# Kernel optimization log

Hardware: AMD Instinct MI355X
Metric: run time of the kernel (lower is better)

The kernel has to match this reference:

```python
import jax, jax.numpy as jnp
import numpy as np

E = 1024   # embed_dim
H = 16     # num_heads
NQ = 8     # ffn_dim == n_qubits
B, S = 2, 2048


def setup_inputs() -> dict:
    key = jax.random.key(0)
    ks = jax.random.split(key, 8)
    g = lambda k, sh, sc=1.0: jax.random.normal(k, sh, jnp.float32) * sc
    return {
        "x": g(ks[0], (B, S, E)),
        "w_qkv": g(ks[1], (3 * E, E), 0.02),      # nn.Linear(E, 3E, bias=False).weight
        "w_comb": g(ks[2], (E, E), 0.02),          # combine Linear weight
        "b_comb": jnp.zeros((E,), jnp.float32),
        "gamma1": jnp.ones((E,), jnp.float32),     # norm1
        "beta1": jnp.zeros((E,), jnp.float32),
        "gamma2": jnp.ones((E,), jnp.float32),     # norm2
        "beta2": jnp.zeros((E,), jnp.float32),
        "theta": g(ks[3], (NQ,)),                  # trainable RY angles
        "w1": g(ks[4], (1, NQ), 0.3),              # linear1 weight [1, n_qubits]
        "b1": jnp.zeros((1,), jnp.float32),
    }


def _layernorm(x, g, b, eps=1e-5):
    m = jnp.mean(x, axis=-1, keepdims=True)
    v = jnp.var(x, axis=-1, keepdims=True)
    return (x - m) * jax.lax.rsqrt(v + eps) * g + b


def reference(x, w_qkv, w_comb, b_comb, gamma1, beta1, gamma2, beta2, theta, w1, b1):
    Bx, Sx, Em = x.shape
    dk = Em // H
    # ---- attention ----
    qkv = (x @ w_qkv.T).reshape(Bx, Sx, 3, H, dk)
    q = jnp.transpose(qkv[:, :, 0], (0, 2, 1, 3))  # [B,H,S,dk]
    k = jnp.transpose(qkv[:, :, 1], (0, 2, 1, 3))
    v = jnp.transpose(qkv[:, :, 2], (0, 2, 1, 3))
    scores = jnp.einsum('bhqd,bhkd->bhqk', q, k) / jnp.sqrt(jnp.float32(dk))
    probs = jax.nn.softmax(scores, axis=-1)        # dropout = identity (eval)
    out = jnp.einsum('bhqk,bhkd->bhqd', probs, v)
    out = jnp.transpose(out, (0, 2, 1, 3)).reshape(Bx, Sx, Em)
    attn = out @ w_comb.T + b_comb
    x1 = _layernorm(x + attn, gamma1, beta1)
    # ---- quantum FFN: RX(x_i) encode, RY(theta_i), <Z_i> = cos(theta_i)*cos(x_i) ----
    z = jnp.cos(x1[..., :theta.shape[0]]) * jnp.cos(theta)  # [B,S,NQ]
    ffn = z @ w1.T + b1                                      # [B,S,1], broadcasts
    return _layernorm(x1 + ffn, gamma2, beta2)
```

## Files before the change

kernel.cpp:

```cpp
#include <hip/hip_runtime.h>
#include <hip/hip_bf16.h>
#include <math.h>

typedef __bf16 bf16;
typedef bf16 bf16x8 __attribute__((ext_vector_type(8)));
typedef float f32x4 __attribute__((ext_vector_type(4)));
typedef unsigned int u32;

#define EMB 1024
#define NH 16
#define DK 64
#define SEQ 2048
#define NB 2
#define NTOK (NB*SEQ)

#define QSCALE 0.18033688011112043f

#if defined(__has_builtin)
#if __has_builtin(__builtin_amdgcn_exp2f)
#define EXP2(x) __builtin_amdgcn_exp2f(x)
#else
#define EXP2(x) exp2f(x)
#endif
#else
#define EXP2(x) exp2f(x)
#endif

__device__ __forceinline__ void gl_lds16(const void* g, void* l) {
    __builtin_amdgcn_global_load_lds(
        (const __attribute__((address_space(1))) u32*)g,
        (__attribute__((address_space(3))) u32*)l, 16, 0, 0);
}

#define SWZ(row, colblk) (((row)*64) + ((((colblk) ^ ((row)&7)))*8))

#define PSTR 72

__global__ __launch_bounds__(256) void convert3(
    const float* __restrict__ s0, const float* __restrict__ s1,
    const float* __restrict__ s2,
    bf16* __restrict__ d0, bf16* __restrict__ d1, bf16* __restrict__ d2)
{
    const float* src; bf16* dst; int n;
    switch (blockIdx.y) {
        case 0:  src = s0; dst = d0; n = NTOK*EMB;  break;
        case 1:  src = s1; dst = d1; n = 3*EMB*EMB; break;
        default: src = s2; dst = d2; n = EMB*EMB;   break;
    }
    int i = (blockIdx.x * 256 + threadIdx.x) * 4;
    if (i + 3 < n) {
        float4 v = *(const float4*)(src + i);
        dst[i+0] = (bf16)v.x; dst[i+1] = (bf16)v.y;
        dst[i+2] = (bf16)v.z; dst[i+3] = (bf16)v.w;
    }
}

template<int MODE, int BM>
__global__ __launch_bounds__(256) void gemm_bt(
    const bf16* __restrict__ Aa, const bf16* __restrict__ Bb,
    bf16* __restrict__ qb, bf16* __restrict__ kb, bf16* __restrict__ vtb,
    float* __restrict__ outc, int Kdim)
{
    constexpr int MI = BM / 32;
    __shared__ __align__(16) bf16 At[BM*64];
    __shared__ __align__(16) bf16 Bt[128*64];
    const int tid  = threadIdx.x;
    const int w    = tid >> 6, lane = tid & 63;
    const int quad = lane >> 4, l15 = lane & 15;
    const int wr   = w >> 1,   wc  = w & 1;
    const int m0 = blockIdx.y * BM, n0 = blockIdx.x * 128;
    const int lrow = lane >> 3;
    const int lswz = ((lane & 7) ^ lrow) * 8;

    f32x4 acc[MI][4] = {};

    for (int k0 = 0; k0 < Kdim; k0 += 64) {
        __syncthreads();
        for (int i = 0; i < MI; ++i) {
            int r = w*(BM/4) + i*8 + lrow;
            gl_lds16(Aa + (size_t)(m0 + r)*Kdim + k0 + lswz, At + (w*(BM/4) + i*8)*64);
        }
        for (int i = 0; i < 4; ++i) {
            int r = w*32 + i*8 + lrow;
            gl_lds16(Bb + (size_t)(n0 + r)*Kdim + k0 + lswz, Bt + (w*32 + i*8)*64);
        }
        __syncthreads();
        for (int kk = 0; kk < 2; ++kk) {
            bf16x8 a[MI], b[4];
            for (int i = 0; i < MI; ++i) {
                int row = wr*(BM/2) + i*16 + l15;
                a[i] = *(const bf16x8*)(At + SWZ(row, 4*kk + quad));
            }
            for (int j = 0; j < 4; ++j) {
                int row = wc*64 + j*16 + l15;
                b[j] = *(const bf16x8*)(Bt + SWZ(row, 4*kk + quad));
            }
            for (int i = 0; i < MI; ++i)
                for (int j = 0; j < 4; ++j)
                    acc[i][j] = __builtin_amdgcn_mfma_f32_16x16x32_bf16(a[i], b[j], acc[i][j], 0, 0, 0);
        }
    }

    for (int i = 0; i < MI; ++i) for (int j = 0; j < 4; ++j) {
        int rb  = m0 + wr*(BM/2) + i*16 + quad*4;
        int col = n0 + wc*64 + j*16 + l15;
        if (MODE == 0) {
            int c = col >> 10, h = (col >> 6) & 15, d = col & 63;
            int b_ = rb >> 11, s = rb & 2047;
            int bh = b_*NH + h;
            if (c == 2) {
                bf16 tmp[4] __attribute__((aligned(8)));
                for (int r = 0; r < 4; ++r) tmp[r] = (bf16)acc[i][j][r];
                *(ushort4*)(vtb + ((size_t)bh*DK + d)*SEQ + s) = *(ushort4*)tmp;
            } else if (c == 0) {
                for (int r = 0; r < 4; ++r)
                    qb[((size_t)bh*SEQ + s + r)*DK + d] = (bf16)(acc[i][j][r] * QSCALE);
            } else {
                for (int r = 0; r < 4; ++r)
                    kb[((size_t)bh*SEQ + s + r)*DK + d] = (bf16)acc[i][j][r];
            }
        } else {
            for (int r = 0; r < 4; ++r)
                outc[(size_t)(rb + r)*EMB + col] = acc[i][j][r];
        }
    }
}

__global__ __launch_bounds__(256) void attn_kernel(
    const bf16* __restrict__ q, const bf16* __restrict__ k,
    const bf16* __restrict__ vt, bf16* __restrict__ out)
{
    __shared__ __align__(16) bf16 QP[4*32*PSTR];
    __shared__ __align__(16) bf16 Kt0[64*64];
    __shared__ __align__(16) bf16 Kt1[64*64];
    __shared__ __align__(16) bf16 Vt0[64*64];
    __shared__ __align__(16) bf16 Vt1[64*64];

    const int tid  = threadIdx.x;
    const int w    = tid >> 6, lane = tid & 63;
    const int quad = lane >> 4, l15 = lane & 15;
    const int bh = blockIdx.y, qt = blockIdx.x;
    const int lrow = lane >> 3;
    const int lswz = ((lane & 7) ^ lrow) * 8;

    for (int i = 0; i < 4; ++i) {
        int r = w*32 + i*8 + lrow;
        gl_lds16(q + ((size_t)bh*SEQ + qt*128 + r)*DK + lswz, QP + (w*32 + i*8)*64);
    }
    asm volatile("s_waitcnt vmcnt(0)" ::: "memory");

    bf16x8 qf[2][2];
    for (int rt = 0; rt < 2; ++rt)
        for (int kk = 0; kk < 2; ++kk)
            qf[rt][kk] = *(const bf16x8*)(QP + SWZ(w*32 + rt*16 + l15, 4*kk + quad));

    bf16* Pw = QP + w * 32 * PSTR;

    f32x4 O[2][4] = {};
    float psum[2][4] = {};

    auto stage_kv = [&](int kt, bf16* Kb, bf16* Vb) {
        for (int i = 0; i < 2; ++i) {
            int r = w*16 + i*8 + lrow;
            gl_lds16(k  + ((size_t)bh*SEQ + kt*64 + r)*DK + lswz, Kb + (w*16 + i*8)*64);
            gl_lds16(vt + ((size_t)bh*DK + r)*SEQ + kt*64 + lswz, Vb + (w*16 + i*8)*64);
        }
    };

    auto compute = [&](const bf16* Kb, const bf16* Vb) {
        f32x4 sc[2][4] = {};
        for (int kk = 0; kk < 2; ++kk)
            for (int j = 0; j < 4; ++j) {
                bf16x8 b = *(const bf16x8*)(Kb + SWZ(j*16 + l15, 4*kk + quad));
                for (int rt = 0; rt < 2; ++rt)
                    sc[rt][j] = __builtin_amdgcn_mfma_f32_16x16x32_bf16(qf[rt][kk], b, sc[rt][j], 0, 0, 0);
            }
        for (int rt = 0; rt < 2; ++rt)
            for (int j = 0; j < 4; ++j)
                for (int r = 0; r < 4; ++r) {
                    float p = EXP2(sc[rt][j][r]);
                    psum[rt][r] += p;
                    Pw[(rt*16 + quad*4 + r)*PSTR + j*16 + l15] = (bf16)p;
                }
        asm volatile("s_waitcnt lgkmcnt(0)" ::: "memory");
        for (int kk = 0; kk < 2; ++kk) {
            bf16x8 vb[4];
            for (int j = 0; j < 4; ++j)
                vb[j] = *(const bf16x8*)(Vb + SWZ(j*16 + l15, 4*kk + quad));
            for (int rt = 0; rt < 2; ++rt) {
                bf16x8 a = *(const bf16x8*)(Pw + (rt*16 + l15)*PSTR + kk*32 + quad*8);
                for (int j = 0; j < 4; ++j)
                    O[rt][j] = __builtin_amdgcn_mfma_f32_16x16x32_bf16(a, vb[j], O[rt][j], 0, 0, 0);
            }
        }
    };

    stage_kv(0, Kt0, Vt0);
    for (int kt2 = 0; kt2 < SEQ/128; ++kt2) {
        __syncthreads();
        stage_kv(2*kt2 + 1, Kt1, Vt1);
        compute(Kt0, Vt0);
        __syncthreads();
        if (kt2 + 1 < SEQ/128)
            stage_kv(2*kt2 + 2, Kt0, Vt0);
        compute(Kt1, Vt1);
    }

    for (int rt = 0; rt < 2; ++rt)
        for (int r = 0; r < 4; ++r) {
            float s = psum[rt][r];
            for (int m = 1; m < 16; m <<= 1) s += __shfl_xor(s, m, 64);
            psum[rt][r] = 1.f / s;
        }

    const int b_ = bh >> 4, h = bh & 15;
    for (int rt = 0; rt < 2; ++rt)
        for (int j = 0; j < 4; ++j)
            for (int r = 0; r < 4; ++r) {
                int t   = b_*SEQ + qt*128 + w*32 + rt*16 + quad*4 + r;
                int col = h*DK + j*16 + l15;
                out[(size_t)t*EMB + col] = (bf16)(O[rt][j][r] * psum[rt][r]);
            }
}

__global__ __launch_bounds__(256) void ln_kernel(
    const float* __restrict__ x, const float* __restrict__ comb,
    const float* __restrict__ bcomb,
    const float* __restrict__ g1, const float* __restrict__ be1,
    const float* __restrict__ g2, const float* __restrict__ be2,
    const float* __restrict__ theta, const float* __restrict__ w1v,
    const float* __restrict__ b1v, float* __restrict__ out)
{
    const int t = blockIdx.x, tid = threadIdx.x;
    __shared__ float red[8];
    __shared__ float fp2[2];
    const int e0 = tid*4;

    float4 xv = *(const float4*)(x    + (size_t)t*EMB + e0);
    float4 cv = *(const float4*)(comb + (size_t)t*EMB + e0);
    float4 bv = *(const float4*)(bcomb + e0);
    float r[4] = { xv.x + cv.x + bv.x, xv.y + cv.y + bv.y,
                   xv.z + cv.z + bv.z, xv.w + cv.w + bv.w };

    float s = 0.f, ss = 0.f;
    for (int i = 0; i < 4; ++i) { s += r[i]; ss += r[i]*r[i]; }
    for (int m = 1; m < 64; m <<= 1) { s += __shfl_xor(s, m, 64); ss += __shfl_xor(ss, m, 64); }
    if ((tid & 63) == 0) { red[(tid>>6)*2] = s; red[(tid>>6)*2+1] = ss; }
    __syncthreads();
    s  = red[0] + red[2] + red[4] + red[6];
    ss = red[1] + red[3] + red[5] + red[7];
    float mean = s * (1.f/1024.f);
    float var  = ss * (1.f/1024.f) - mean*mean;
    float inv  = rsqrtf(var + 1e-5f);
    float x1[4];
    for (int i = 0; i < 4; ++i) {
        int e = e0 + i;
        x1[i] = (r[i] - mean)*inv*g1[e] + be1[e];
    }
    __syncthreads();
    if (e0 < 8) {
        float pf = 0.f;
        for (int i = 0; i < 4; ++i) {
            int e = e0 + i;
            pf += cosf(x1[i]) * cosf(theta[e]) * w1v[e];
        }
        fp2[tid] = pf;
    }
    __syncthreads();
    float f = fp2[0] + fp2[1] + b1v[0];

    float s2 = 0.f, ss2 = 0.f;
    for (int i = 0; i < 4; ++i) { float v2 = x1[i] + f; s2 += v2; ss2 += v2*v2; }
    for (int m = 1; m < 64; m <<= 1) { s2 += __shfl_xor(s2, m, 64); ss2 += __shfl_xor(ss2, m, 64); }
    if ((tid & 63) == 0) { red[(tid>>6)*2] = s2; red[(tid>>6)*2+1] = ss2; }
    __syncthreads();
    s2  = red[0] + red[2] + red[4] + red[6];
    ss2 = red[1] + red[3] + red[5] + red[7];
    float mean2 = s2 * (1.f/1024.f);
    float var2  = ss2 * (1.f/1024.f) - mean2*mean2;
    float inv2  = rsqrtf(var2 + 1e-5f);
    float4 ov;
    ov.x = ((x1[0] + f) - mean2)*inv2*g2[e0+0] + be2[e0+0];
    ov.y = ((x1[1] + f) - mean2)*inv2*g2[e0+1] + be2[e0+1];
    ov.z = ((x1[2] + f) - mean2)*inv2*g2[e0+2] + be2[e0+2];
    ov.w = ((x1[3] + f) - mean2)*inv2*g2[e0+3] + be2[e0+3];
    *(float4*)(out + (size_t)t*EMB + e0) = ov;
}

extern "C" void kernel_launch(void* const* d_in, const int* in_sizes, int n_in,
                              void* d_out, int out_size, void* d_ws, size_t ws_size,
                              hipStream_t stream)
{
    const float* x      = (const float*)d_in[0];
    const float* w_qkv  = (const float*)d_in[1];
    const float* w_comb = (const float*)d_in[2];
    const float* b_comb = (const float*)d_in[3];
    const float* g1     = (const float*)d_in[4];
    const float* be1    = (const float*)d_in[5];
    const float* g2     = (const float*)d_in[6];
    const float* be2    = (const float*)d_in[7];
    const float* theta  = (const float*)d_in[8];
    const float* w1v    = (const float*)d_in[9];
    const float* b1v    = (const float*)d_in[10];
    float* out = (float*)d_out;

    char* ws = (char*)d_ws;
    bf16*  xb     = (bf16*)(ws);
    bf16*  wqkvb  = (bf16*)(ws + ( 8u<<20));
    bf16*  wcombb = (bf16*)(ws + (14u<<20));
    bf16*  qb     = (bf16*)(ws + (16u<<20));
    bf16*  kb     = (bf16*)(ws + (24u<<20));
    bf16*  vtb    = (bf16*)(ws + (32u<<20));
    bf16*  attn   = (bf16*)(ws + (40u<<20));
    float* comb   = (float*)(ws + (16u<<20));

    convert3<<<dim3(4096, 3), 256, 0, stream>>>(x, w_qkv, w_comb, xb, wqkvb, wcombb);

    gemm_bt<0,128><<<dim3(3*EMB/128, NTOK/128), 256, 0, stream>>>(
        xb, wqkvb, qb, kb, vtb, nullptr, EMB);
    attn_kernel<<<dim3(SEQ/128, NB*NH), 256, 0, stream>>>(qb, kb, vtb, attn);
    gemm_bt<1,64><<<dim3(EMB/128, NTOK/64), 256, 0, stream>>>(
        attn, wcombb, nullptr, nullptr, nullptr, comb, EMB);
    ln_kernel<<<NTOK, 256, 0, stream>>>(x, comb, b_comb, g1, be1, g2, be2,
                                        theta, w1v, b1v, out);
}
```

Baseline: 215.9 us.

## Split attention key range across two blocks and add reduction kernel

The attention grid is doubled so each block processes half of the key sequence. Each half writes unnormalized bf16 partial outputs and per-row exp-sums, and a new reduce kernel sums the two halves and normalizes. The goal is more blocks in flight and better CU occupancy on the attention stage. In exchange it adds an extra launch, extra global traffic for the partial outputs, and bf16 rounding of unnormalized partials.

```diff
diff --git a/kernel.cpp b/kernel.cpp
--- a/kernel.cpp
+++ b/kernel.cpp
@@ -128,7 +128,8 @@
 
 __global__ __launch_bounds__(256) void attn_kernel(
     const bf16* __restrict__ q, const bf16* __restrict__ k,
-    const bf16* __restrict__ vt, bf16* __restrict__ out)
+    const bf16* __restrict__ vt,
+    bf16* __restrict__ o0, bf16* __restrict__ o1, float* __restrict__ psb)
 {
     __shared__ __align__(16) bf16 QP[4*32*PSTR];
     __shared__ __align__(16) bf16 Kt0[64*64];
@@ -139,9 +140,11 @@
     const int tid  = threadIdx.x;
     const int w    = tid >> 6, lane = tid & 63;
     const int quad = lane >> 4, l15 = lane & 15;
-    const int bh = blockIdx.y, qt = blockIdx.x;
+    const int bh = blockIdx.y;
+    const int qt = blockIdx.x & 15, part = blockIdx.x >> 4;
     const int lrow = lane >> 3;
     const int lswz = ((lane & 7) ^ lrow) * 8;
+    const int kt0base = part * (SEQ/128);
 
     for (int i = 0; i < 4; ++i) {
         int r = w*32 + i*8 + lrow;
@@ -195,14 +198,14 @@
         }
     };
 
-    stage_kv(0, Kt0, Vt0);
-    for (int kt2 = 0; kt2 < SEQ/128; ++kt2) {
+    stage_kv(kt0base, Kt0, Vt0);
+    for (int kt2 = 0; kt2 < SEQ/256; ++kt2) {
         __syncthreads();
-        stage_kv(2*kt2 + 1, Kt1, Vt1);
+        stage_kv(kt0base + 2*kt2 + 1, Kt1, Vt1);
         compute(Kt0, Vt0);
         __syncthreads();
-        if (kt2 + 1 < SEQ/128)
-            stage_kv(2*kt2 + 2, Kt0, Vt0);
+        if (kt2 + 1 < SEQ/256)
+            stage_kv(kt0base + 2*kt2 + 2, Kt0, Vt0);
         compute(Kt1, Vt1);
     }
 
@@ -210,17 +213,45 @@
         for (int r = 0; r < 4; ++r) {
             float s = psum[rt][r];
             for (int m = 1; m < 16; m <<= 1) s += __shfl_xor(s, m, 64);
-            psum[rt][r] = 1.f / s;
-        }
-
+            psum[rt][r] = s;
+        }
+    if (l15 == 0) {
+        for (int rt = 0; rt < 2; ++rt)
+            for (int r = 0; r < 4; ++r) {
+                int row = qt*128 + w*32 + rt*16 + quad*4 + r;
+                psb[(size_t)(part*NB*NH + bh)*SEQ + row] = psum[rt][r];
+            }
+    }
+
+    bf16* opart = part ? o1 : o0;
     const int b_ = bh >> 4, h = bh & 15;
     for (int rt = 0; rt < 2; ++rt)
         for (int j = 0; j < 4; ++j)
             for (int r = 0; r < 4; ++r) {
                 int t   = b_*SEQ + qt*128 + w*32 + rt*16 + quad*4 + r;
                 int col = h*DK + j*16 + l15;
-                out[(size_t)t*EMB + col] = (bf16)(O[rt][j][r] * psum[rt][r]);
-            }
+                opart[(size_t)t*EMB + col] = (bf16)O[rt][j][r];
+            }
+}
+
+__global__ __launch_bounds__(256) void attn_reduce(
+    const bf16* __restrict__ o0, const bf16* __restrict__ o1,
+    const float* __restrict__ psb, bf16* __restrict__ outa)
+{
+    const int t = blockIdx.x, tid = threadIdx.x;
+    const int e0 = tid * 4;
+    const int h = e0 >> 6, b_ = t >> 11, s = t & 2047;
+    const int bh = b_*NH + h;
+    float ps = psb[(size_t)bh*SEQ + s] + psb[(size_t)(NB*NH + bh)*SEQ + s];
+    float inv = 1.f / ps;
+    ushort4 a = *(const ushort4*)((const unsigned short*)o0 + (size_t)t*EMB + e0);
+    ushort4 c = *(const ushort4*)((const unsigned short*)o1 + (size_t)t*EMB + e0);
+    const bf16* ap = (const bf16*)&a;
+    const bf16* cp = (const bf16*)&c;
+    bf16 r[4] __attribute__((aligned(8)));
+    for (int i = 0; i < 4; ++i)
+        r[i] = (bf16)(((float)ap[i] + (float)cp[i]) * inv);
+    *(ushort4*)((unsigned short*)outa + (size_t)t*EMB + e0) = *(ushort4*)r;
 }
 
 __global__ __launch_bounds__(256) void ln_kernel(
@@ -313,12 +344,16 @@
     bf16*  vtb    = (bf16*)(ws + (32u<<20));
     bf16*  attn   = (bf16*)(ws + (40u<<20));
     float* comb   = (float*)(ws + (16u<<20));
+    bf16*  opart0 = xb;
+    float* psb    = (float*)(ws + (13u<<20));
 
     convert3<<<dim3(4096, 3), 256, 0, stream>>>(x, w_qkv, w_comb, xb, wqkvb, wcombb);
 
     gemm_bt<0,128><<<dim3(3*EMB/128, NTOK/128), 256, 0, stream>>>(
         xb, wqkvb, qb, kb, vtb, nullptr, EMB);
-    attn_kernel<<<dim3(SEQ/128, NB*NH), 256, 0, stream>>>(qb, kb, vtb, attn);
+    attn_kernel<<<dim3(2*SEQ/128, NB*NH), 256, 0, stream>>>(
+        qb, kb, vtb, opart0, attn, psb);
+    attn_reduce<<<NTOK, 256, 0, stream>>>(opart0, attn, psb, attn);
     gemm_bt<1,64><<<dim3(EMB/128, NTOK/64), 256, 0, stream>>>(
         attn, wcombb, nullptr, nullptr, nullptr, comb, EMB);
     ln_kernel<<<NTOK, 256, 0, stream>>>(x, comb, b_comb, g1, be1, g2, be2,
```

New measurement: 224.6 us. +4.0%, slower.
